# Kernel optimization log

Measured on AMD Instinct MI355X. Metric: run time of the kernel, lower is better.

Reference implementation:

```python
import jax, jax.numpy as jnp
import numpy as np

N_USERS = 30000
N_ENT = 70000
N = N_USERS + N_ENT          # total graph nodes
E = 1_600_000                # edges (avg degree 16)
D = 64                       # embed_dim
B = 4096                     # scored user-item pairs
LEAKY_SLOPE = 0.01           # torch nn.LeakyReLU default
EPS = 1e-12                  # torch F.normalize default eps


def setup_inputs() -> dict:
    key = jax.random.key(0)
    ks = jax.random.split(key, 16)
    inp = {
        "edge_row": jax.random.randint(ks[0], (E,), 0, N, dtype=jnp.int32),
        "edge_col": jax.random.randint(ks[1], (E,), 0, N, dtype=jnp.int32),
        "edge_vals": jax.random.uniform(ks[2], (E,), dtype=jnp.float32) / 16.0,
        "user_embed": jax.random.normal(ks[3], (N_USERS, D), jnp.float32) * 0.1,
        "entity_embed": jax.random.normal(ks[4], (N_ENT, D), jnp.float32) * 0.1,
        "W1_0": jax.random.normal(ks[5], (D, 64), jnp.float32) * (1.0 / np.sqrt(D)),
        "b1_0": jnp.zeros((64,), jnp.float32),
        "W2_0": jax.random.normal(ks[6], (D, 64), jnp.float32) * (1.0 / np.sqrt(D)),
        "b2_0": jnp.zeros((64,), jnp.float32),
        "W1_1": jax.random.normal(ks[7], (64, 32), jnp.float32) * (1.0 / 8.0),
        "b1_1": jnp.zeros((32,), jnp.float32),
        "W2_1": jax.random.normal(ks[8], (64, 32), jnp.float32) * (1.0 / 8.0),
        "b2_1": jnp.zeros((32,), jnp.float32),
        "user_ids": jax.random.randint(ks[9], (B,), 0, N_USERS, dtype=jnp.int32),
        "item_ids": jax.random.randint(ks[10], (B,), 0, N_ENT, dtype=jnp.int32),
    }
    return inp


def _gnn_layer(feats, edge_row, edge_col, edge_vals, W1, b1, W2, b2):
    # sparse adj @ feats  ==  scatter-add of weighted source features to rows
    gathered = feats[edge_col] * edge_vals[:, None]          # (E, d_in)
    h_neigh = jax.ops.segment_sum(gathered, edge_row, num_segments=N)  # (N, d_in)
    term1 = (feats + h_neigh) @ W1 + b1
    term2 = (feats * h_neigh) @ W2 + b2
    h = jax.nn.leaky_relu(term1 + term2, negative_slope=LEAKY_SLOPE)
    # F.normalize(h, p=2, dim=1)
    norm = jnp.linalg.norm(h, axis=1, keepdims=True)
    return h / jnp.maximum(norm, EPS)


def reference(edge_row, edge_col, edge_vals, user_embed, entity_embed,
              W1_0, b1_0, W2_0, b2_0, W1_1, b1_1, W2_1, b2_1,
              user_ids, item_ids):
    a0 = jnp.concatenate([user_embed, entity_embed], axis=0)     # (N, 64)
    a1 = _gnn_layer(a0, edge_row, edge_col, edge_vals, W1_0, b1_0, W2_0, b2_0)  # (N, 64)
    a2 = _gnn_layer(a1, edge_row, edge_col, edge_vals, W1_1, b1_1, W2_1, b2_1)  # (N, 32)
    final = jnp.concatenate([a0, a1, a2], axis=1)                # (N, 160)
    u = final[user_ids]                                          # (B, 160)
    i = final[N_USERS + item_ids]                                # (B, 160)
    return jnp.sum(u * i, axis=1)                                # (B,)
```

## Files before the change

kernel.cpp:

```cpp
#include <hip/hip_runtime.h>
#include <hip/hip_bf16.h>
#include <math.h>

#define LEAKY 0.01f
#define SCAN_BLOCK 256
#define SCAN_ITEMS 4
#define SCAN_TILE (SCAN_BLOCK * SCAN_ITEMS)

struct __align__(8) Bf4 { __hip_bfloat16 a, b, c, d; };

__global__ void count_edges(const int* __restrict__ row, int E,
                            int* __restrict__ deg, int* __restrict__ rank) {
    int i = blockIdx.x * blockDim.x + threadIdx.x;
    if (i < E) rank[i] = atomicAdd(&deg[row[i]], 1);
}

__global__ __launch_bounds__(SCAN_BLOCK) void scan_phase1(
    const int* __restrict__ deg, int* __restrict__ blocksum, int N) {
    __shared__ int red[SCAN_BLOCK];
    int b = blockIdx.x, t = threadIdx.x;
    int base = b * SCAN_TILE + t * SCAN_ITEMS;
    int s = 0;
#pragma unroll
    for (int j = 0; j < SCAN_ITEMS; j++) {
        int i = base + j;
        if (i < N) s += deg[i];
    }
    red[t] = s;
    __syncthreads();
    for (int off = SCAN_BLOCK / 2; off > 0; off >>= 1) {
        if (t < off) red[t] += red[t + off];
        __syncthreads();
    }
    if (t == 0) blocksum[b] = red[0];
}

__global__ __launch_bounds__(1024) void scan_phase2(
    const int* __restrict__ blocksum, int* __restrict__ blockoff,
    int* __restrict__ row_ptr, int G, int N) {
    __shared__ int sums[1024];
    int t = threadIdx.x;
    sums[t] = (t < G) ? blocksum[t] : 0;
    __syncthreads();
    for (int off = 1; off < 1024; off <<= 1) {
        int v = (t >= off) ? sums[t - off] : 0;
        __syncthreads();
        sums[t] += v;
        __syncthreads();
    }
    if (t < G) blockoff[t] = (t == 0) ? 0 : sums[t - 1];
    if (t == G - 1) row_ptr[N] = sums[t];
}

__global__ __launch_bounds__(SCAN_BLOCK) void scan_phase3(
    const int* __restrict__ deg, const int* __restrict__ blockoff,
    int* __restrict__ row_ptr, int N) {
    __shared__ int red[SCAN_BLOCK];
    int b = blockIdx.x, t = threadIdx.x;
    int base = b * SCAN_TILE + t * SCAN_ITEMS;
    int v[SCAN_ITEMS];
    int s = 0;
#pragma unroll
    for (int j = 0; j < SCAN_ITEMS; j++) {
        int i = base + j;
        v[j] = (i < N) ? deg[i] : 0;
        s += v[j];
    }
    red[t] = s;
    __syncthreads();
    for (int off = 1; off < SCAN_BLOCK; off <<= 1) {
        int x = (t >= off) ? red[t - off] : 0;
        __syncthreads();
        red[t] += x;
        __syncthreads();
    }
    int run = blockoff[b] + ((t == 0) ? 0 : red[t - 1]);
#pragma unroll
    for (int j = 0; j < SCAN_ITEMS; j++) {
        int i = base + j;
        if (i < N) { row_ptr[i] = run; run += v[j]; }
    }
}

__global__ void build_a0(const float4* __restrict__ ue, const float4* __restrict__ ee,
                         float4* __restrict__ a0, __hip_bfloat16* __restrict__ a0b,
                         int nu4, int ntot4) {
    int i = blockIdx.x * blockDim.x + threadIdx.x;
    if (i < ntot4) {
        float4 v = (i < nu4) ? ue[i] : ee[i - nu4];
        a0[i] = v;
        Bf4 q = {__float2bfloat16(v.x), __float2bfloat16(v.y),
                 __float2bfloat16(v.z), __float2bfloat16(v.w)};
        *(Bf4*)&a0b[(size_t)i * 4] = q;
    }
}

__global__ void fill_csr(const int* __restrict__ row, const int* __restrict__ col,
                         const float* __restrict__ val, const int* __restrict__ rank,
                         const int* __restrict__ row_ptr, int E,
                         int2* __restrict__ csr) {
    int i = blockIdx.x * blockDim.x + threadIdx.x;
    if (i < E) {
        int p = row_ptr[row[i]] + rank[i];
        csr[p] = make_int2(col[i], __float_as_int(val[i]));
    }
}

__device__ __forceinline__ void fma4(float o[4], float sv, const float4& wv) {
    o[0] = fmaf(sv, wv.x, o[0]);
    o[1] = fmaf(sv, wv.y, o[1]);
    o[2] = fmaf(sv, wv.z, o[2]);
    o[3] = fmaf(sv, wv.w, o[3]);
}

template<int DOUT>
__global__ __launch_bounds__(256, 8) void gnn_layer(
    const float* __restrict__ feats, const __hip_bfloat16* __restrict__ featsb,
    const int2* __restrict__ csr, const int* __restrict__ row_ptr,
    const float* __restrict__ W1, const float* __restrict__ b1,
    const float* __restrict__ W2, const float* __restrict__ b2,
    float* __restrict__ out, __hip_bfloat16* __restrict__ outb, int N) {
    __shared__ __align__(16) float S[32 * 132];
    int wv = threadIdx.x >> 6, lane = threadIdx.x & 63;
    int nb = blockIdx.x * 32 + wv * 8;
    int sl = lane & 31;
    int selbase = lane & 32;

    int rp_l = row_ptr[min(nb + min(lane, 8), N)];
    int e0[8], dg[8];
#pragma unroll
    for (int ni = 0; ni < 8; ni++) {
        int a = __builtin_amdgcn_readlane(rp_l, ni);
        int b = __builtin_amdgcn_readlane(rp_l, ni + 1);
        e0[ni] = a; dg[ni] = b - a;
    }

    const uint* fb2 = (const uint*)featsb;
    const float2* f2 = (const float2*)feats;

#pragma unroll
    for (int pr = 0; pr < 4; pr++) {
        int nA = nb + 2 * pr, nB = nA + 1;
        int myNode = selbase ? nB : nA;
        int myE0   = selbase ? e0[2 * pr + 1] : e0[2 * pr];
        int myDg   = selbase ? dg[2 * pr + 1] : dg[2 * pr];
        int mx = max(dg[2 * pr], dg[2 * pr + 1]);
        float2 x = f2[(size_t)min(myNode, N - 1) * 32 + sl];
        float accx = 0.f, accy = 0.f;
        for (int done = 0; done < mx; done += 32) {
            int2 m = make_int2(0, 0);
            if (sl < myDg - done) m = csr[myE0 + done + sl];
            int lim = min(mx - done, 32);
            for (int c = 0; c < lim; c += 8) {
                uint w[8]; float vv[8];
#pragma unroll
                for (int u = 0; u < 8; u++) {
                    int j = c + u;
                    int col = __shfl(m.x, selbase + j, 64);
                    vv[u] = __int_as_float(__shfl(m.y, selbase + j, 64));
                    w[u] = fb2[(size_t)col * 32 + sl];
                }
#pragma unroll
                for (int u = 0; u < 8; u++) {
                    accx = fmaf(vv[u], __uint_as_float(w[u] << 16), accx);
                    accy = fmaf(vv[u], __uint_as_float(w[u] & 0xffff0000u), accy);
                }
            }
        }
        if (myNode < N) {
            float* sp = &S[(wv * 8 + 2 * pr + (selbase ? 1 : 0)) * 132];
            *(float2*)&sp[2 * sl]      = make_float2(x.x + accx, x.y + accy);
            *(float2*)&sp[64 + 2 * sl] = make_float2(x.x * accx, x.y * accy);
        }
    }
    __threadfence_block();

    if constexpr (DOUT == 64) {
        int strip = lane & 15, g = lane >> 4;
        int d0 = strip * 4;
        float4 b1v = *(const float4*)&b1[d0];
        float4 b2v = *(const float4*)&b2[d0];
        float oa[4] = {b1v.x + b2v.x, b1v.y + b2v.y, b1v.z + b2v.z, b1v.w + b2v.w};
        float ob[4] = {oa[0], oa[1], oa[2], oa[3]};
        const float* spa = &S[(wv * 8 + 2 * g) * 132];
        const float* spb = spa + 132;
#pragma unroll
        for (int half = 0; half < 2; half++) {
            const float* W  = half ? W2 : W1;
            const float* sa = spa + half * 64;
            const float* sb = spb + half * 64;
#pragma unroll 2
            for (int k = 0; k < 64; k += 4) {
                float4 va = *(const float4*)&sa[k];
                float4 vb = *(const float4*)&sb[k];
                float4 wr0 = *(const float4*)&W[(k + 0) * 64 + d0];
                float4 wr1 = *(const float4*)&W[(k + 1) * 64 + d0];
                float4 wr2 = *(const float4*)&W[(k + 2) * 64 + d0];
                float4 wr3 = *(const float4*)&W[(k + 3) * 64 + d0];
                fma4(oa, va.x, wr0); fma4(oa, va.y, wr1);
                fma4(oa, va.z, wr2); fma4(oa, va.w, wr3);
                fma4(ob, vb.x, wr0); fma4(ob, vb.y, wr1);
                fma4(ob, vb.z, wr2); fma4(ob, vb.w, wr3);
            }
        }
#pragma unroll
        for (int t = 0; t < 2; t++) {
            float* o = t ? ob : oa;
            float h0 = (o[0] > 0.f) ? o[0] : LEAKY * o[0];
            float h1 = (o[1] > 0.f) ? o[1] : LEAKY * o[1];
            float h2 = (o[2] > 0.f) ? o[2] : LEAKY * o[2];
            float h3 = (o[3] > 0.f) ? o[3] : LEAKY * o[3];
            float ss = h0 * h0 + h1 * h1 + h2 * h2 + h3 * h3;
            ss += __shfl_xor(ss, 1, 64);
            ss += __shfl_xor(ss, 2, 64);
            ss += __shfl_xor(ss, 4, 64);
            ss += __shfl_xor(ss, 8, 64);
            float sc = 1.0f / fmaxf(sqrtf(ss), 1e-12f);
            int node = nb + 2 * g + t;
            if (node < N) {
                float4 r = {h0 * sc, h1 * sc, h2 * sc, h3 * sc};
                *(float4*)&out[(size_t)node * 64 + d0] = r;
                Bf4 q = {__float2bfloat16(r.x), __float2bfloat16(r.y),
                         __float2bfloat16(r.z), __float2bfloat16(r.w)};
                *(Bf4*)&outb[(size_t)node * 64 + d0] = q;
            }
        }
    } else {
        int strip = lane & 7, nI = lane >> 3;
        int d0 = strip * 4;
        float4 b1v = *(const float4*)&b1[d0];
        float4 b2v = *(const float4*)&b2[d0];
        float o[4] = {b1v.x + b2v.x, b1v.y + b2v.y, b1v.z + b2v.z, b1v.w + b2v.w};
        const float* sp = &S[(wv * 8 + nI) * 132];
#pragma unroll
        for (int half = 0; half < 2; half++) {
            const float* W  = half ? W2 : W1;
            const float* sv = sp + half * 64;
#pragma unroll 2
            for (int k = 0; k < 64; k += 4) {
                float4 v   = *(const float4*)&sv[k];
                float4 wr0 = *(const float4*)&W[(k + 0) * 32 + d0];
                float4 wr1 = *(const float4*)&W[(k + 1) * 32 + d0];
                float4 wr2 = *(const float4*)&W[(k + 2) * 32 + d0];
                float4 wr3 = *(const float4*)&W[(k + 3) * 32 + d0];
                fma4(o, v.x, wr0); fma4(o, v.y, wr1);
                fma4(o, v.z, wr2); fma4(o, v.w, wr3);
            }
        }
        float h0 = (o[0] > 0.f) ? o[0] : LEAKY * o[0];
        float h1 = (o[1] > 0.f) ? o[1] : LEAKY * o[1];
        float h2 = (o[2] > 0.f) ? o[2] : LEAKY * o[2];
        float h3 = (o[3] > 0.f) ? o[3] : LEAKY * o[3];
        float ss = h0 * h0 + h1 * h1 + h2 * h2 + h3 * h3;
        ss += __shfl_xor(ss, 1, 64);
        ss += __shfl_xor(ss, 2, 64);
        ss += __shfl_xor(ss, 4, 64);
        float sc = 1.0f / fmaxf(sqrtf(ss), 1e-12f);
        int node = nb + nI;
        if (node < N) {
            float4 r = {h0 * sc, h1 * sc, h2 * sc, h3 * sc};
            *(float4*)&out[(size_t)node * 32 + d0] = r;
        }
    }
}

__global__ __launch_bounds__(256) void score_pairs(
    const float* __restrict__ a0, const float* __restrict__ a1,
    const float* __restrict__ a2,
    const int* __restrict__ uid, const int* __restrict__ iid,
    float* __restrict__ out, int B, int NU) {
    int wave = threadIdx.x >> 6, lane = threadIdx.x & 63;
    int p = blockIdx.x * 4 + wave;
    if (p >= B) return;
    int u = uid[p], it = iid[p];
    size_t un = (size_t)u, in = (size_t)(NU + it);
    float s = a0[un * 64 + lane] * a0[in * 64 + lane];
    s = fmaf(a1[un * 64 + lane], a1[in * 64 + lane], s);
    if (lane < 32) s = fmaf(a2[un * 32 + lane], a2[in * 32 + lane], s);
#pragma unroll
    for (int m = 32; m >= 1; m >>= 1) s += __shfl_xor(s, m, 64);
    if (lane == 0) out[p] = s;
}

extern "C" void kernel_launch(void* const* d_in, const int* in_sizes, int n_in,
                              void* d_out, int out_size, void* d_ws, size_t ws_size,
                              hipStream_t stream) {
    const int*   edge_row  = (const int*)d_in[0];
    const int*   edge_col  = (const int*)d_in[1];
    const float* edge_vals = (const float*)d_in[2];
    const float* ue        = (const float*)d_in[3];
    const float* ee        = (const float*)d_in[4];
    const float* W1_0 = (const float*)d_in[5];
    const float* b1_0 = (const float*)d_in[6];
    const float* W2_0 = (const float*)d_in[7];
    const float* b2_0 = (const float*)d_in[8];
    const float* W1_1 = (const float*)d_in[9];
    const float* b1_1 = (const float*)d_in[10];
    const float* W2_1 = (const float*)d_in[11];
    const float* b2_1 = (const float*)d_in[12];
    const int*   uid  = (const int*)d_in[13];
    const int*   iid  = (const int*)d_in[14];
    float* out = (float*)d_out;

    const int E  = in_sizes[0];
    const int NU = in_sizes[3] / 64;
    const int NE = in_sizes[4] / 64;
    const int N  = NU + NE;
    const int B  = in_sizes[13];
    const int G  = (N + SCAN_TILE - 1) / SCAN_TILE;

    char* ws = (char*)d_ws;
    size_t off = 0;
    auto alloc = [&](size_t bytes) -> char* {
        char* p = ws + off;
        off = (off + bytes + 255) & ~(size_t)255;
        return p;
    };
    int*   deg      = (int*)alloc((size_t)N * 4);
    int*   rank     = (int*)alloc((size_t)E * 4);
    int*   row_ptr  = (int*)alloc((size_t)(N + 1) * 4);
    int*   blocksum = (int*)alloc((size_t)1024 * 4);
    int*   blockoff = (int*)alloc((size_t)1024 * 4);
    int2*  csr      = (int2*)alloc((size_t)E * 8);
    float* a0       = (float*)alloc((size_t)N * 64 * 4);
    float* a1       = (float*)alloc((size_t)N * 64 * 4);
    float* a2       = (float*)alloc((size_t)N * 32 * 4);
    __hip_bfloat16* a0b = (__hip_bfloat16*)alloc((size_t)N * 64 * 2);
    __hip_bfloat16* a1b = (__hip_bfloat16*)alloc((size_t)N * 64 * 2);
    (void)ws_size; (void)n_in; (void)out_size; (void)NE;

    hipMemsetAsync(deg, 0, (size_t)N * 4, stream);
    count_edges<<<(E + 255) / 256, 256, 0, stream>>>(edge_row, E, deg, rank);
    scan_phase1<<<G, SCAN_BLOCK, 0, stream>>>(deg, blocksum, N);
    scan_phase2<<<1, 1024, 0, stream>>>(blocksum, blockoff, row_ptr, G, N);
    scan_phase3<<<G, SCAN_BLOCK, 0, stream>>>(deg, blockoff, row_ptr, N);
    fill_csr<<<(E + 255) / 256, 256, 0, stream>>>(edge_row, edge_col, edge_vals,
                                                  rank, row_ptr, E, csr);
    int ntot4 = N * 16, nu4 = NU * 16;
    build_a0<<<(ntot4 + 255) / 256, 256, 0, stream>>>((const float4*)ue, (const float4*)ee,
                                                      (float4*)a0, a0b, nu4, ntot4);
    gnn_layer<64><<<(N + 31) / 32, 256, 0, stream>>>(a0, a0b, csr, row_ptr,
                                                     W1_0, b1_0, W2_0, b2_0, a1, a1b, N);
    gnn_layer<32><<<(N + 31) / 32, 256, 0, stream>>>(a1, a1b, csr, row_ptr,
                                                     W1_1, b1_1, W2_1, b2_1, a2, nullptr, N);
    score_pairs<<<(B + 3) / 4, 256, 0, stream>>>(a0, a1, a2, uid, iid, out, B, NU);
}
```

Baseline: 393.8 us.

## Drop fp32 a0 copy and prefetch first CSR chunk and self features per node pair

The fp32 concatenated a0 buffer is removed. Layer 0 and the scorer now read the user and entity embeddings directly, and the build kernel writes only the bf16 copy. In the GNN layer, the first 32-edge CSR chunk and the self feature for all four node pairs are loaded up front, before any gather loop starts, so these loads overlap instead of sitting serialized inside each pair's loop. This saves a 25.6MB write plus reads, at the cost of extra registers, which may reduce occupancy under the launch bounds.

After: 379.2 us. -3.7%, faster.

```diff
diff --git a/kernel.cpp b/kernel.cpp
--- a/kernel.cpp
+++ b/kernel.cpp
@@ -82,13 +82,11 @@
     }
 }
 
-__global__ void build_a0(const float4* __restrict__ ue, const float4* __restrict__ ee,
-                         float4* __restrict__ a0, __hip_bfloat16* __restrict__ a0b,
-                         int nu4, int ntot4) {
+__global__ void build_a0b(const float4* __restrict__ ue, const float4* __restrict__ ee,
+                          __hip_bfloat16* __restrict__ a0b, int nu4, int ntot4) {
     int i = blockIdx.x * blockDim.x + threadIdx.x;
     if (i < ntot4) {
         float4 v = (i < nu4) ? ue[i] : ee[i - nu4];
-        a0[i] = v;
         Bf4 q = {__float2bfloat16(v.x), __float2bfloat16(v.y),
                  __float2bfloat16(v.z), __float2bfloat16(v.w)};
         *(Bf4*)&a0b[(size_t)i * 4] = q;
@@ -115,7 +113,8 @@
 
 template<int DOUT>
 __global__ __launch_bounds__(256, 8) void gnn_layer(
-    const float* __restrict__ feats, const __hip_bfloat16* __restrict__ featsb,
+    const float* __restrict__ featsU, const float* __restrict__ featsE, int NUo,
+    const __hip_bfloat16* __restrict__ featsb,
     const int2* __restrict__ csr, const int* __restrict__ row_ptr,
     const float* __restrict__ W1, const float* __restrict__ b1,
     const float* __restrict__ W2, const float* __restrict__ b2,
@@ -136,41 +135,70 @@
     }
 
     const uint* fb2 = (const uint*)featsb;
-    const float2* f2 = (const float2*)feats;
-
+    const float2* f2u = (const float2*)featsU;
+    const float2* f2e = (const float2*)featsE;
+
+    int2 m0[4];
+    float2 xv[4];
 #pragma unroll
     for (int pr = 0; pr < 4; pr++) {
-        int nA = nb + 2 * pr, nB = nA + 1;
-        int myNode = selbase ? nB : nA;
-        int myE0   = selbase ? e0[2 * pr + 1] : e0[2 * pr];
-        int myDg   = selbase ? dg[2 * pr + 1] : dg[2 * pr];
+        int idx = 2 * pr + (selbase ? 1 : 0);
+        int myDg = dg[idx], myE0 = e0[idx];
+        m0[pr] = make_int2(0, 0);
+        if (sl < min(myDg, 32)) m0[pr] = csr[myE0 + sl];
+        int nn = min(nb + idx, N - 1);
+        xv[pr] = (nn < NUo) ? f2u[(size_t)nn * 32 + sl]
+                            : f2e[(size_t)(nn - NUo) * 32 + sl];
+    }
+
+#pragma unroll
+    for (int pr = 0; pr < 4; pr++) {
+        int idx = 2 * pr + (selbase ? 1 : 0);
+        int myDg = dg[idx], myE0 = e0[idx];
         int mx = max(dg[2 * pr], dg[2 * pr + 1]);
-        float2 x = f2[(size_t)min(myNode, N - 1) * 32 + sl];
         float accx = 0.f, accy = 0.f;
-        for (int done = 0; done < mx; done += 32) {
-            int2 m = make_int2(0, 0);
-            if (sl < myDg - done) m = csr[myE0 + done + sl];
-            int lim = min(mx - done, 32);
-            for (int c = 0; c < lim; c += 8) {
-                uint w[8]; float vv[8];
-#pragma unroll
-                for (int u = 0; u < 8; u++) {
-                    int j = c + u;
-                    int col = __shfl(m.x, selbase + j, 64);
-                    vv[u] = __int_as_float(__shfl(m.y, selbase + j, 64));
-                    w[u] = fb2[(size_t)col * 32 + sl];
+        int lim = min(mx, 32);
+        for (int c = 0; c < lim; c += 8) {
+            uint w[8]; float vv[8];
+#pragma unroll
+            for (int u = 0; u < 8; u++) {
+                int j = c + u;
+                int col = __shfl(m0[pr].x, selbase + j, 64);
+                vv[u] = __int_as_float(__shfl(m0[pr].y, selbase + j, 64));
+                w[u] = fb2[(size_t)col * 32 + sl];
+            }
+#pragma unroll
+            for (int u = 0; u < 8; u++) {
+                accx = fmaf(vv[u], __uint_as_float(w[u] << 16), accx);
+                accy = fmaf(vv[u], __uint_as_float(w[u] & 0xffff0000u), accy);
+            }
+        }
+        if (mx > 32) {
+            for (int done = 32; done < mx; done += 32) {
+                int2 mt = make_int2(0, 0);
+                if (sl < myDg - done) mt = csr[myE0 + done + sl];
+                int lim2 = min(mx - done, 32);
+                for (int c = 0; c < lim2; c += 8) {
+                    uint w[8]; float vv[8];
+#pragma unroll
+                    for (int u = 0; u < 8; u++) {
+                        int j = c + u;
+                        int col = __shfl(mt.x, selbase + j, 64);
+                        vv[u] = __int_as_float(__shfl(mt.y, selbase + j, 64));
+                        w[u] = fb2[(size_t)col * 32 + sl];
+                    }
+#pragma unroll
+                    for (int u = 0; u < 8; u++) {
+                        accx = fmaf(vv[u], __uint_as_float(w[u] << 16), accx);
+                        accy = fmaf(vv[u], __uint_as_float(w[u] & 0xffff0000u), accy);
+                    }
                 }
-#pragma unroll
-                for (int u = 0; u < 8; u++) {
-                    accx = fmaf(vv[u], __uint_as_float(w[u] << 16), accx);
-                    accy = fmaf(vv[u], __uint_as_float(w[u] & 0xffff0000u), accy);
-                }
-            }
-        }
-        if (myNode < N) {
-            float* sp = &S[(wv * 8 + 2 * pr + (selbase ? 1 : 0)) * 132];
-            *(float2*)&sp[2 * sl]      = make_float2(x.x + accx, x.y + accy);
-            *(float2*)&sp[64 + 2 * sl] = make_float2(x.x * accx, x.y * accy);
+            }
+        }
+        if (nb + idx < N) {
+            float* sp = &S[(wv * 8 + idx) * 132];
+            *(float2*)&sp[2 * sl]      = make_float2(xv[pr].x + accx, xv[pr].y + accy);
+            *(float2*)&sp[64 + 2 * sl] = make_float2(xv[pr].x * accx, xv[pr].y * accy);
         }
     }
     __threadfence_block();
@@ -265,8 +293,8 @@
 }
 
 __global__ __launch_bounds__(256) void score_pairs(
-    const float* __restrict__ a0, const float* __restrict__ a1,
-    const float* __restrict__ a2,
+    const float* __restrict__ ue, const float* __restrict__ ee,
+    const float* __restrict__ a1, const float* __restrict__ a2,
     const int* __restrict__ uid, const int* __restrict__ iid,
     float* __restrict__ out, int B, int NU) {
     int wave = threadIdx.x >> 6, lane = threadIdx.x & 63;
@@ -274,7 +302,7 @@
     if (p >= B) return;
     int u = uid[p], it = iid[p];
     size_t un = (size_t)u, in = (size_t)(NU + it);
-    float s = a0[un * 64 + lane] * a0[in * 64 + lane];
+    float s = ue[un * 64 + lane] * ee[(size_t)it * 64 + lane];
     s = fmaf(a1[un * 64 + lane], a1[in * 64 + lane], s);
     if (lane < 32) s = fmaf(a2[un * 32 + lane], a2[in * 32 + lane], s);
 #pragma unroll
@@ -322,7 +350,6 @@
     int*   blocksum = (int*)alloc((size_t)1024 * 4);
     int*   blockoff = (int*)alloc((size_t)1024 * 4);
     int2*  csr      = (int2*)alloc((size_t)E * 8);
-    float* a0       = (float*)alloc((size_t)N * 64 * 4);
     float* a1       = (float*)alloc((size_t)N * 64 * 4);
     float* a2       = (float*)alloc((size_t)N * 32 * 4);
     __hip_bfloat16* a0b = (__hip_bfloat16*)alloc((size_t)N * 64 * 2);
@@ -337,11 +364,11 @@
     fill_csr<<<(E + 255) / 256, 256, 0, stream>>>(edge_row, edge_col, edge_vals,
                                                   rank, row_ptr, E, csr);
     int ntot4 = N * 16, nu4 = NU * 16;
-    build_a0<<<(ntot4 + 255) / 256, 256, 0, stream>>>((const float4*)ue, (const float4*)ee,
-                                                      (float4*)a0, a0b, nu4, ntot4);
-    gnn_layer<64><<<(N + 31) / 32, 256, 0, stream>>>(a0, a0b, csr, row_ptr,
+    build_a0b<<<(ntot4 + 255) / 256, 256, 0, stream>>>((const float4*)ue, (const float4*)ee,
+                                                       a0b, nu4, ntot4);
+    gnn_layer<64><<<(N + 31) / 32, 256, 0, stream>>>(ue, ee, NU, a0b, csr, row_ptr,
                                                      W1_0, b1_0, W2_0, b2_0, a1, a1b, N);
-    gnn_layer<32><<<(N + 31) / 32, 256, 0, stream>>>(a1, a1b, csr, row_ptr,
+    gnn_layer<32><<<(N + 31) / 32, 256, 0, stream>>>(a1, a1, N, a1b, csr, row_ptr,
                                                      W1_1, b1_1, W2_1, b2_1, a2, nullptr, N);
-    score_pairs<<<(B + 3) / 4, 256, 0, stream>>>(a0, a1, a2, uid, iid, out, B, NU);
-}
+    score_pairs<<<(B + 3) / 4, 256, 0, stream>>>(ue, ee, a1, a2, uid, iid, out, B, NU);
+}
```
